# Kernel tuning notes

Measured on AMD Instinct MI355X. Metric: run time of the kernel, lower is better.

## Reference

```python
import jax, jax.numpy as jnp
import numpy as np

N_NODES = 100000
N_EDGES = 1600000
D = 64
H = 128
EPS = 0.0  # learn_eps=False


def setup_inputs() -> dict:
    key = jax.random.key(0)
    k1, k2, k3, k4 = jax.random.split(key, 4)
    x = jax.random.normal(k1, (N_NODES, D), dtype=jnp.float32)
    edge_index = jax.random.randint(k2, (2, N_EDGES), 0, N_NODES, dtype=jnp.int64)
    W1 = jax.random.normal(k3, (D, H), dtype=jnp.float32) * (1.0 / np.sqrt(D))
    b1 = jnp.zeros((H,), dtype=jnp.float32)
    W2 = jax.random.normal(k4, (H, D), dtype=jnp.float32) * (1.0 / np.sqrt(H))
    b2 = jnp.zeros((D,), dtype=jnp.float32)
    return {"x": x, "edge_index": edge_index, "W1": W1, "b1": b1, "W2": W2, "b2": b2}


def reference(x, edge_index, W1, b1, W2, b2):
    src, dst = edge_index[0], edge_index[1]
    # gather neighbor features and scatter-add to destination nodes
    agg = jax.ops.segment_sum(x[src], dst, num_segments=N_NODES)  # [N, D]
    out = agg + (1.0 + EPS) * x
    # GIN MLP: Linear -> ReLU -> Linear
    h = jax.nn.relu(out @ W1 + b1)
    return h @ W2 + b2
```

## Files before the change

kernel.cpp:

```cpp
#include <hip/hip_runtime.h>

#define N_NODES 100000
#define N_EDGES 1600000
#define D 64
#define H 128
#define SCAN_BS 512
#define SCAN_NBLK ((N_NODES + SCAN_BS - 1) / SCAN_BS)

#define NB 1563
#define NCHUNK 256
#define EPC (N_EDGES / NCHUNK)
#define BCAP 2560
#define OVF_CAP 4096

#define MFMA_GRID 512
#define SH_STRIDE 132

typedef __attribute__((ext_vector_type(8))) short short8;
typedef __attribute__((ext_vector_type(4))) float floatx4;
typedef __attribute__((ext_vector_type(4))) unsigned short ushort4_t;

__device__ __forceinline__ unsigned short f2bf(float f) {
    unsigned u = __builtin_bit_cast(unsigned, f);
    u += 0x7FFFu + ((u >> 16) & 1u);
    return (unsigned short)(u >> 16);
}
__device__ __forceinline__ float bf2f(unsigned short u) {
    unsigned v = ((unsigned)u) << 16;
    return __builtin_bit_cast(float, v);
}

__global__ __launch_bounds__(256) void k_zero(int* __restrict__ p, int n) {
    int i = blockIdx.x * 256 + threadIdx.x;
    if (i < n) p[i] = 0;
}

__global__ __launch_bounds__(256) void k_xbf16(const float4* __restrict__ x4,
                                               ushort4_t* __restrict__ y, int n4) {
    int i = blockIdx.x * 256 + threadIdx.x;
    if (i >= n4) return;
    float4 v = x4[i];
    ushort4_t o;
    o[0] = f2bf(v.x); o[1] = f2bf(v.y); o[2] = f2bf(v.z); o[3] = f2bf(v.w);
    y[i] = o;
}

__global__ __launch_bounds__(256) void k_bhist(const int* __restrict__ dst,
                                               int* __restrict__ M2,
                                               int* __restrict__ ovfn) {
    __shared__ int hist[NB];
    int t = threadIdx.x, c = blockIdx.x;
    if (c == 0 && t == 0) ovfn[0] = 0;
    for (int i = t; i < NB; i += 256) hist[i] = 0;
    __syncthreads();
    const int* dp = dst + c * EPC;
    for (int i = t; i < EPC; i += 256) atomicAdd(&hist[dp[i] >> 6], 1);
    __syncthreads();
    int* mp = M2 + c * NB;
    for (int i = t; i < NB; i += 256) mp[i] = hist[i];
}

__global__ __launch_bounds__(256) void k_colscan(int* __restrict__ M2,
                                                 int* __restrict__ colsum) {
    int b = blockIdx.x * 256 + threadIdx.x;
    if (b >= NB) return;
    int run = 0;
    for (int c = 0; c < NCHUNK; c++) {
        int v = M2[c * NB + b];
        M2[c * NB + b] = run;
        run += v;
    }
    colsum[b] = run;
}

__global__ __launch_bounds__(512) void k_bscan(const int* __restrict__ colsum,
                                               int* __restrict__ bends) {
    __shared__ int part[512];
    int t = threadIdx.x;
    int i0 = t * 4;
    int v0 = (i0 + 0 < NB) ? colsum[i0 + 0] : 0;
    int v1 = (i0 + 1 < NB) ? colsum[i0 + 1] : 0;
    int v2 = (i0 + 2 < NB) ? colsum[i0 + 2] : 0;
    int v3 = (i0 + 3 < NB) ? colsum[i0 + 3] : 0;
    int r0 = v0, r1 = r0 + v1, r2 = r1 + v2, r3 = r2 + v3;
    part[t] = r3;
    __syncthreads();
    for (int off = 1; off < 512; off <<= 1) {
        int u = (t >= off) ? part[t - off] : 0;
        __syncthreads();
        part[t] += u;
        __syncthreads();
    }
    int base = (t > 0) ? part[t - 1] : 0;
    if (i0 + 0 < NB) bends[i0 + 0] = base + r0;
    if (i0 + 1 < NB) bends[i0 + 1] = base + r1;
    if (i0 + 2 < NB) bends[i0 + 2] = base + r2;
    if (i0 + 3 < NB) bends[i0 + 3] = base + r3;
}

__global__ __launch_bounds__(256) void k_part(const int* __restrict__ src,
                                              const int* __restrict__ dst,
                                              const int* __restrict__ M2,
                                              const int* __restrict__ bends,
                                              int* __restrict__ ebuf) {
    __shared__ int cur[NB];
    int t = threadIdx.x, c = blockIdx.x;
    const int* mp = M2 + c * NB;
    for (int i = t; i < NB; i += 256)
        cur[i] = ((i > 0) ? bends[i - 1] : 0) + mp[i];
    __syncthreads();
    const int* sp = src + c * EPC;
    const int* dp = dst + c * EPC;
    for (int i = t; i < EPC; i += 256) {
        int d = dp[i], s = sp[i];
        int p = atomicAdd(&cur[d >> 6], 1);
        ebuf[p] = s | ((d & 63) << 17);
    }
}

__global__ __launch_bounds__(256) void k_bagg3(const float* __restrict__ x,
                                               const unsigned short* __restrict__ x16,
                                               const int* __restrict__ ebuf,
                                               const int* __restrict__ bends,
                                               int* __restrict__ ovfn,
                                               int* __restrict__ ovf,
                                               float* __restrict__ out) {
    __shared__ int scur[64];
    __shared__ int snd[64];
    __shared__ int slist[BCAP];
    int t = threadIdx.x, b = blockIdx.x;
    int estart = (b > 0) ? bends[b - 1] : 0;
    int ne = bends[b] - estart;
    const int* ep = ebuf + estart;

    if (t < 64) scur[t] = 0;
    __syncthreads();
    for (int i = t; i < ne; i += 256) atomicAdd(&scur[ep[i] >> 17], 1);
    __syncthreads();
    if (t < 64) {
        int v = scur[t], s = v;
#pragma unroll
        for (int off = 1; off < 64; off <<= 1) {
            int u = __shfl_up(s, off, 64);
            if (t >= off) s += u;
        }
        snd[t] = s;
        scur[t] = s - v;
    }
    __syncthreads();
    for (int i = t; i < ne; i += 256) {
        int v = ep[i];
        int p = atomicAdd(&scur[v >> 17], 1);
        if (p < BCAP) {
            slist[p] = v & 0x1FFFF;
        } else {
            int o = atomicAdd(ovfn, 1);
            if (o < OVF_CAP) { ovf[2 * o] = b * 64 + (v >> 17); ovf[2 * o + 1] = v & 0x1FFFF; }
        }
    }
    __syncthreads();

    int qw = t >> 4;
    int f4 = t & 15;
#pragma unroll
    for (int k = 0; k < 4; k++) {
        int dlow = qw * 4 + k;
        int node = b * 64 + dlow;
        int s0 = (dlow > 0) ? snd[dlow - 1] : 0;
        int e1 = snd[dlow];
        if (s0 > BCAP) s0 = BCAP;
        if (e1 > BCAP) e1 = BCAP;
        float4 a0 = make_float4(0.f, 0.f, 0.f, 0.f);
        float4 a1 = a0, a2 = a0, a3 = a0;
        int i = s0;
        for (; i + 4 <= e1; i += 4) {
            int sA = slist[i], sB = slist[i + 1], sC = slist[i + 2], sD = slist[i + 3];
            ushort4_t uA = *(const ushort4_t*)&x16[(size_t)sA * D + f4 * 4];
            ushort4_t uB = *(const ushort4_t*)&x16[(size_t)sB * D + f4 * 4];
            ushort4_t uC = *(const ushort4_t*)&x16[(size_t)sC * D + f4 * 4];
            ushort4_t uD = *(const ushort4_t*)&x16[(size_t)sD * D + f4 * 4];
            a0.x += bf2f(uA[0]); a0.y += bf2f(uA[1]); a0.z += bf2f(uA[2]); a0.w += bf2f(uA[3]);
            a1.x += bf2f(uB[0]); a1.y += bf2f(uB[1]); a1.z += bf2f(uB[2]); a1.w += bf2f(uB[3]);
            a2.x += bf2f(uC[0]); a2.y += bf2f(uC[1]); a2.z += bf2f(uC[2]); a2.w += bf2f(uC[3]);
            a3.x += bf2f(uD[0]); a3.y += bf2f(uD[1]); a3.z += bf2f(uD[2]); a3.w += bf2f(uD[3]);
        }
        for (; i < e1; i++) {
            int sA = slist[i];
            ushort4_t uA = *(const ushort4_t*)&x16[(size_t)sA * D + f4 * 4];
            a0.x += bf2f(uA[0]); a0.y += bf2f(uA[1]); a0.z += bf2f(uA[2]); a0.w += bf2f(uA[3]);
        }
        a0.x = (a0.x + a1.x) + (a2.x + a3.x);
        a0.y = (a0.y + a1.y) + (a2.y + a3.y);
        a0.z = (a0.z + a1.z) + (a2.z + a3.z);
        a0.w = (a0.w + a1.w) + (a2.w + a3.w);
        if (node < N_NODES) {
            float4 xv = *(const float4*)&x[(size_t)node * D + f4 * 4];
            float4 o;
            o.x = a0.x + xv.x; o.y = a0.y + xv.y; o.z = a0.z + xv.z; o.w = a0.w + xv.w;
            *(float4*)&out[(size_t)node * D + f4 * 4] = o;
        }
    }
}

__global__ __launch_bounds__(256) void k_ovf(const int* __restrict__ ovfn,
                                             const int* __restrict__ ovf,
                                             const float* __restrict__ x,
                                             float* __restrict__ out) {
    int n = *ovfn;
    if (n > OVF_CAP) n = OVF_CAP;
    int f = threadIdx.x & 63;
    for (int idx = threadIdx.x >> 6; idx < n; idx += 4) {
        int d = ovf[2 * idx], s = ovf[2 * idx + 1];
        atomicAdd(&out[(size_t)d * D + f], x[(size_t)s * D + f]);
    }
}

__global__ __launch_bounds__(SCAN_BS) void k_scan1(const int* __restrict__ cnt,
                                                   int* __restrict__ ends,
                                                   int* __restrict__ bsum, int n) {
    __shared__ int s[SCAN_BS];
    int t = threadIdx.x, b = blockIdx.x;
    int id = b * SCAN_BS + t;
    s[t] = (id < n) ? cnt[id] : 0;
    __syncthreads();
    for (int off = 1; off < SCAN_BS; off <<= 1) {
        int u = (t >= off) ? s[t - off] : 0;
        __syncthreads();
        s[t] += u;
        __syncthreads();
    }
    if (id < n) ends[id] = s[t];
    if (t == SCAN_BS - 1) bsum[b] = s[t];
}

__global__ __launch_bounds__(256) void k_scan2(int* __restrict__ bsum, int nb) {
    __shared__ int s[256];
    int t = threadIdx.x;
    s[t] = (t < nb) ? bsum[t] : 0;
    __syncthreads();
    for (int off = 1; off < 256; off <<= 1) {
        int u = (t >= off) ? s[t - off] : 0;
        __syncthreads();
        s[t] += u;
        __syncthreads();
    }
    if (t < nb) bsum[t] = s[t];
}

__global__ __launch_bounds__(SCAN_BS) void k_scan3(int* __restrict__ ends,
                                                   const int* __restrict__ bsum, int n) {
    int t = threadIdx.x, b = blockIdx.x;
    int id = b * SCAN_BS + t;
    if (b > 0 && id < n) ends[id] += bsum[b - 1];
}

__global__ __launch_bounds__(256) void k_histpos(const int* __restrict__ dst,
                                                 int* __restrict__ cnt,
                                                 int* __restrict__ pos) {
    int e = blockIdx.x * 256 + threadIdx.x;
    if (e < N_EDGES) pos[e] = atomicAdd(&cnt[dst[e]], 1);
}

__global__ __launch_bounds__(256) void k_fill2(const int* __restrict__ src,
                                               const int* __restrict__ dst,
                                               const int* __restrict__ pos,
                                               const int* __restrict__ ends,
                                               int* __restrict__ csr) {
    int e = blockIdx.x * 256 + threadIdx.x;
    if (e >= N_EDGES) return;
    int d = dst[e];
    int start = (d > 0) ? ends[d - 1] : 0;
    csr[start + pos[e]] = src[e];
}

__global__ __launch_bounds__(256) void k_agg(const float* __restrict__ x,
                                             const int* __restrict__ csr,
                                             const int* __restrict__ ends,
                                             float* __restrict__ out) {
    int node = blockIdx.x * 4 + (threadIdx.x >> 6);
    if (node >= N_NODES) return;
    int f = threadIdx.x & 63;
    int start = (node > 0) ? ends[node - 1] : 0;
    int end = ends[node];
    float a0 = x[(size_t)node * D + f], a1 = 0.f, a2 = 0.f, a3 = 0.f;
    int e = start;
    for (; e + 4 <= end; e += 4) {
        int s0 = csr[e], s1 = csr[e + 1], s2 = csr[e + 2], s3 = csr[e + 3];
        a0 += x[(size_t)s0 * D + f];
        a1 += x[(size_t)s1 * D + f];
        a2 += x[(size_t)s2 * D + f];
        a3 += x[(size_t)s3 * D + f];
    }
    for (; e < end; e++) a0 += x[(size_t)csr[e] * D + f];
    out[(size_t)node * D + f] = (a0 + a1) + (a2 + a3);
}

__global__ __launch_bounds__(256) void k_init(const float4* __restrict__ x4,
                                              float4* __restrict__ agg4, int n4) {
    int i = blockIdx.x * 256 + threadIdx.x;
    if (i < n4) agg4[i] = x4[i];
}

__global__ __launch_bounds__(256) void k_scatter(const float4* __restrict__ x4,
                                                 const int* __restrict__ src,
                                                 const int* __restrict__ dst,
                                                 float* __restrict__ agg) {
    int gid = blockIdx.x * 256 + threadIdx.x;
    int e = gid >> 4;
    if (e >= N_EDGES) return;
    int c = gid & 15;
    float4 v = x4[src[e] * 16 + c];
    float* p = agg + (size_t)dst[e] * D + c * 4;
    atomicAdd(p + 0, v.x);
    atomicAdd(p + 1, v.y);
    atomicAdd(p + 2, v.z);
    atomicAdd(p + 3, v.w);
}

__global__ __launch_bounds__(256) void k_mlp_mfma(float* __restrict__ io,
                                                  const float* __restrict__ W1,
                                                  const float* __restrict__ b1,
                                                  const float* __restrict__ W2,
                                                  const float* __restrict__ b2) {
    __shared__ unsigned short sW1b[8192];
    __shared__ unsigned short sW2b[8192];
    __shared__ float sh[4][16 * SH_STRIDE];
    __shared__ float sb1[H];
    __shared__ float sb2[D];

    int t = threadIdx.x;

    for (int q = t; q < 8192; q += 256) {
        int j = q & 7, l = (q >> 3) & 63, f = q >> 9;
        int nt = f & 7, kt = f >> 3;
        int k = kt * 32 + ((l >> 4) << 3) + j;
        int n = nt * 16 + (l & 15);
        sW1b[q] = f2bf(W1[k * H + n]);
    }
    for (int q = t; q < 8192; q += 256) {
        int j = q & 7, l = (q >> 3) & 63, f = q >> 9;
        int nt = f & 3, kt = f >> 2;
        int k = kt * 32 + ((l >> 4) << 3) + j;
        int n = nt * 16 + (l & 15);
        sW2b[q] = f2bf(W2[k * D + n]);
    }
    if (t < H) sb1[t] = b1[t];
    if (t >= H && t < H + D) sb2[t - H] = b2[t - H];
    __syncthreads();

    int w = t >> 6, l = t & 63;
    int m = l & 15, q4 = l >> 4;
    float* shw = sh[w];

    const int NT16 = N_NODES / 16;
    const int WAVES = MFMA_GRID * 4;
    const int ITERS = (NT16 + WAVES - 1) / WAVES;

    for (int it = 0; it < ITERS; ++it) {
        int tl = it * WAVES + blockIdx.x * 4 + w;
        bool valid = tl < NT16;
        int nbase = tl * 16;

        if (valid) {
            const float* xr = io + (size_t)(nbase + m) * D + q4 * 8;
            float4 a0 = *(const float4*)(xr);
            float4 a1 = *(const float4*)(xr + 4);
            float4 c0 = *(const float4*)(xr + 32);
            float4 c1 = *(const float4*)(xr + 36);
            short8 A0, A1;
            A0[0] = f2bf(a0.x); A0[1] = f2bf(a0.y); A0[2] = f2bf(a0.z); A0[3] = f2bf(a0.w);
            A0[4] = f2bf(a1.x); A0[5] = f2bf(a1.y); A0[6] = f2bf(a1.z); A0[7] = f2bf(a1.w);
            A1[0] = f2bf(c0.x); A1[1] = f2bf(c0.y); A1[2] = f2bf(c0.z); A1[3] = f2bf(c0.w);
            A1[4] = f2bf(c1.x); A1[5] = f2bf(c1.y); A1[6] = f2bf(c1.z); A1[7] = f2bf(c1.w);

#pragma unroll
            for (int nt = 0; nt < 8; nt++) {
                float bv = sb1[nt * 16 + m];
                floatx4 acc = {bv, bv, bv, bv};
                short8 B0 = *(const short8*)&sW1b[(0 * 8 + nt) * 512 + l * 8];
                short8 B1 = *(const short8*)&sW1b[(1 * 8 + nt) * 512 + l * 8];
                acc = __builtin_amdgcn_mfma_f32_16x16x32_bf16(A0, B0, acc, 0, 0, 0);
                acc = __builtin_amdgcn_mfma_f32_16x16x32_bf16(A1, B1, acc, 0, 0, 0);
#pragma unroll
                for (int r = 0; r < 4; r++)
                    shw[(q4 * 4 + r) * SH_STRIDE + nt * 16 + m] = fmaxf(acc[r], 0.f);
            }
        }
        __syncthreads();

        if (valid) {
            short8 Ah[4];
#pragma unroll
            for (int kt = 0; kt < 4; kt++) {
                const float* hr = &shw[m * SH_STRIDE + kt * 32 + q4 * 8];
                float4 h0 = *(const float4*)(hr);
                float4 h1 = *(const float4*)(hr + 4);
                Ah[kt][0] = f2bf(h0.x); Ah[kt][1] = f2bf(h0.y);
                Ah[kt][2] = f2bf(h0.z); Ah[kt][3] = f2bf(h0.w);
                Ah[kt][4] = f2bf(h1.x); Ah[kt][5] = f2bf(h1.y);
                Ah[kt][6] = f2bf(h1.z); Ah[kt][7] = f2bf(h1.w);
            }
#pragma unroll
            for (int nt = 0; nt < 4; nt++) {
                float bv = sb2[nt * 16 + m];
                floatx4 acc = {bv, bv, bv, bv};
#pragma unroll
                for (int kt = 0; kt < 4; kt++) {
                    short8 B = *(const short8*)&sW2b[(kt * 4 + nt) * 512 + l * 8];
                    acc = __builtin_amdgcn_mfma_f32_16x16x32_bf16(Ah[kt], B, acc, 0, 0, 0);
                }
#pragma unroll
                for (int r = 0; r < 4; r++)
                    io[(size_t)(nbase + q4 * 4 + r) * D + nt * 16 + m] = acc[r];
            }
        }
        __syncthreads();
    }
}

extern "C" void kernel_launch(void* const* d_in, const int* in_sizes, int n_in,
                              void* d_out, int out_size, void* d_ws, size_t ws_size,
                              hipStream_t stream) {
    const float* x  = (const float*)d_in[0];
    const int* eidx = (const int*)d_in[1];
    const float* W1 = (const float*)d_in[2];
    const float* b1 = (const float*)d_in[3];
    const float* W2 = (const float*)d_in[4];
    const float* b2 = (const float*)d_in[5];
    float* out      = (float*)d_out;

    const int* src = eidx;
    const int* dst = eidx + N_EDGES;

    int ge = (N_EDGES + 255) / 256;
    int n4 = N_NODES * D / 4;

    size_t need_A = (size_t)N_NODES * D * sizeof(unsigned short)
                  + (size_t)(N_EDGES + NCHUNK * NB + 2 * NB + 4 + 2 * OVF_CAP) * sizeof(int);
    size_t need_B = (size_t)(2 * N_NODES + 512 + 2 * N_EDGES) * sizeof(int);

    if (ws_size >= need_A) {
        unsigned short* x16 = (unsigned short*)d_ws;
        int* ebuf   = (int*)(x16 + (size_t)N_NODES * D);
        int* M2     = ebuf + N_EDGES;
        int* colsum = M2 + NCHUNK * NB;
        int* bends  = colsum + NB;
        int* ovfn   = bends + NB;
        int* ovf    = ovfn + 4;

        k_xbf16<<<(n4 + 255) / 256, 256, 0, stream>>>((const float4*)x, (ushort4_t*)x16, n4);
        k_bhist<<<NCHUNK, 256, 0, stream>>>(dst, M2, ovfn);
        k_colscan<<<(NB + 255) / 256, 256, 0, stream>>>(M2, colsum);
        k_bscan<<<1, 512, 0, stream>>>(colsum, bends);
        k_part<<<NCHUNK, 256, 0, stream>>>(src, dst, M2, bends, ebuf);
        k_bagg3<<<NB, 256, 0, stream>>>(x, x16, ebuf, bends, ovfn, ovf, out);
        k_ovf<<<1, 256, 0, stream>>>(ovfn, ovf, x, out);
    } else if (ws_size >= need_B) {
        int* cnt  = (int*)d_ws;
        int* ends = cnt + N_NODES;
        int* bsum = ends + N_NODES;
        int* pos  = bsum + 512;
        int* csr  = pos + N_EDGES;

        k_zero<<<(N_NODES + 255) / 256, 256, 0, stream>>>(cnt, N_NODES);
        k_histpos<<<ge, 256, 0, stream>>>(dst, cnt, pos);
        k_scan1<<<SCAN_NBLK, SCAN_BS, 0, stream>>>(cnt, ends, bsum, N_NODES);
        k_scan2<<<1, 256, 0, stream>>>(bsum, SCAN_NBLK);
        k_scan3<<<SCAN_NBLK, SCAN_BS, 0, stream>>>(ends, bsum, N_NODES);
        k_fill2<<<ge, 256, 0, stream>>>(src, dst, pos, ends, csr);
        k_agg<<<(N_NODES + 3) / 4, 256, 0, stream>>>(x, csr, ends, out);
    } else {
        k_init<<<(n4 + 255) / 256, 256, 0, stream>>>((const float4*)x, (float4*)out, n4);
        long long total = (long long)N_EDGES * 16;
        k_scatter<<<(int)((total + 255) / 256), 256, 0, stream>>>(
            (const float4*)x, src, dst, out);
    }

    k_mlp_mfma<<<MFMA_GRID, 256, 0, stream>>>(out, W1, b1, W2, b2);
}
```

Baseline: 195.6 us.

## Store aggregated features as bf16 and fuse preprocessing kernels into one launch

The aggregation kernel now writes its node features as bf16 into a workspace buffer, so the MLP reads half the bytes and skips per-tile conversion. Hidden activations are kept as bf16 in shared memory. The weight conversion and swizzling runs once in a merged preprocessing kernel that also does the edge histogram and the x-to-bf16 conversion, replacing three launches. The aggregation also uses 8-wide bf16 loads, and the MLP grid grows to 768 blocks. In exchange, rounding the aggregate to bf16 before the MLP adds error, and the overflow path now does non-atomic read-modify-write on bf16 values with a single thread block.

```diff
diff --git a/kernel.cpp b/kernel.cpp
--- a/kernel.cpp
+++ b/kernel.cpp
@@ -13,12 +13,14 @@
 #define BCAP 2560
 #define OVF_CAP 4096
 
-#define MFMA_GRID 512
+#define MFMA_GRID 768
 #define SH_STRIDE 132
+#define SH16_ST 136
 
 typedef __attribute__((ext_vector_type(8))) short short8;
 typedef __attribute__((ext_vector_type(4))) float floatx4;
 typedef __attribute__((ext_vector_type(4))) unsigned short ushort4_t;
+typedef __attribute__((ext_vector_type(8))) unsigned short ushort8_t;
 
 __device__ __forceinline__ unsigned short f2bf(float f) {
     unsigned u = __builtin_bit_cast(unsigned, f);
@@ -35,29 +37,53 @@
     if (i < n) p[i] = 0;
 }
 
-__global__ __launch_bounds__(256) void k_xbf16(const float4* __restrict__ x4,
-                                               ushort4_t* __restrict__ y, int n4) {
-    int i = blockIdx.x * 256 + threadIdx.x;
-    if (i >= n4) return;
-    float4 v = x4[i];
-    ushort4_t o;
-    o[0] = f2bf(v.x); o[1] = f2bf(v.y); o[2] = f2bf(v.z); o[3] = f2bf(v.w);
-    y[i] = o;
-}
-
-__global__ __launch_bounds__(256) void k_bhist(const int* __restrict__ dst,
-                                               int* __restrict__ M2,
-                                               int* __restrict__ ovfn) {
+__global__ __launch_bounds__(256) void k_pre(const float4* __restrict__ x4,
+                                             ushort4_t* __restrict__ y, int n4,
+                                             const int* __restrict__ dst,
+                                             int* __restrict__ M2,
+                                             int* __restrict__ ovfn,
+                                             const float* __restrict__ W1,
+                                             const float* __restrict__ W2,
+                                             unsigned short* __restrict__ gW1b,
+                                             unsigned short* __restrict__ gW2b) {
     __shared__ int hist[NB];
-    int t = threadIdx.x, c = blockIdx.x;
-    if (c == 0 && t == 0) ovfn[0] = 0;
-    for (int i = t; i < NB; i += 256) hist[i] = 0;
-    __syncthreads();
-    const int* dp = dst + c * EPC;
-    for (int i = t; i < EPC; i += 256) atomicAdd(&hist[dp[i] >> 6], 1);
-    __syncthreads();
-    int* mp = M2 + c * NB;
-    for (int i = t; i < NB; i += 256) mp[i] = hist[i];
+    int t = threadIdx.x, blk = blockIdx.x;
+    if (blk < NCHUNK) {
+        int c = blk;
+        if (c == 0 && t == 0) ovfn[0] = 0;
+        for (int i = t; i < NB; i += 256) hist[i] = 0;
+        __syncthreads();
+        const int* dp = dst + c * EPC;
+        for (int i = t; i < EPC; i += 256) atomicAdd(&hist[dp[i] >> 6], 1);
+        __syncthreads();
+        int* mp = M2 + c * NB;
+        for (int i = t; i < NB; i += 256) mp[i] = hist[i];
+    } else if (blk == NCHUNK) {
+        for (int q = t; q < 8192; q += 256) {
+            int j = q & 7, l = (q >> 3) & 63, f = q >> 9;
+            int nt = f & 7, kt = f >> 3;
+            int k = kt * 32 + ((l >> 4) << 3) + j;
+            int n = nt * 16 + (l & 15);
+            gW1b[q] = f2bf(W1[k * H + n]);
+        }
+    } else if (blk == NCHUNK + 1) {
+        for (int q = t; q < 8192; q += 256) {
+            int j = q & 7, l = (q >> 3) & 63, f = q >> 9;
+            int nt = f & 3, kt = f >> 2;
+            int k = kt * 32 + ((l >> 4) << 3) + j;
+            int n = nt * 16 + (l & 15);
+            gW2b[q] = f2bf(W2[k * D + n]);
+        }
+    } else {
+        int cb = blk - NCHUNK - 2;
+        int nconv = gridDim.x - NCHUNK - 2;
+        for (int i = cb * 256 + t; i < n4; i += nconv * 256) {
+            float4 v = x4[i];
+            ushort4_t o;
+            o[0] = f2bf(v.x); o[1] = f2bf(v.y); o[2] = f2bf(v.z); o[3] = f2bf(v.w);
+            y[i] = o;
+        }
+    }
 }
 
 __global__ __launch_bounds__(256) void k_colscan(int* __restrict__ M2,
@@ -118,13 +144,13 @@
     }
 }
 
-__global__ __launch_bounds__(256) void k_bagg3(const float* __restrict__ x,
+__global__ __launch_bounds__(256) void k_bagg4(const float* __restrict__ x,
                                                const unsigned short* __restrict__ x16,
                                                const int* __restrict__ ebuf,
                                                const int* __restrict__ bends,
                                                int* __restrict__ ovfn,
                                                int* __restrict__ ovf,
-                                               float* __restrict__ out) {
+                                               unsigned short* __restrict__ o16) {
     __shared__ int scur[64];
     __shared__ int snd[64];
     __shared__ int slist[BCAP];
@@ -160,58 +186,248 @@
     }
     __syncthreads();
 
-    int qw = t >> 4;
-    int f4 = t & 15;
-#pragma unroll
-    for (int k = 0; k < 4; k++) {
-        int dlow = qw * 4 + k;
+    int g = t >> 3;
+    int l8 = t & 7;
+#pragma unroll
+    for (int k = 0; k < 2; k++) {
+        int dlow = g * 2 + k;
         int node = b * 64 + dlow;
         int s0 = (dlow > 0) ? snd[dlow - 1] : 0;
         int e1 = snd[dlow];
         if (s0 > BCAP) s0 = BCAP;
         if (e1 > BCAP) e1 = BCAP;
-        float4 a0 = make_float4(0.f, 0.f, 0.f, 0.f);
-        float4 a1 = a0, a2 = a0, a3 = a0;
+        float accA[8], accB[8];
+#pragma unroll
+        for (int j = 0; j < 8; j++) { accA[j] = 0.f; accB[j] = 0.f; }
         int i = s0;
         for (; i + 4 <= e1; i += 4) {
             int sA = slist[i], sB = slist[i + 1], sC = slist[i + 2], sD = slist[i + 3];
-            ushort4_t uA = *(const ushort4_t*)&x16[(size_t)sA * D + f4 * 4];
-            ushort4_t uB = *(const ushort4_t*)&x16[(size_t)sB * D + f4 * 4];
-            ushort4_t uC = *(const ushort4_t*)&x16[(size_t)sC * D + f4 * 4];
-            ushort4_t uD = *(const ushort4_t*)&x16[(size_t)sD * D + f4 * 4];
-            a0.x += bf2f(uA[0]); a0.y += bf2f(uA[1]); a0.z += bf2f(uA[2]); a0.w += bf2f(uA[3]);
-            a1.x += bf2f(uB[0]); a1.y += bf2f(uB[1]); a1.z += bf2f(uB[2]); a1.w += bf2f(uB[3]);
-            a2.x += bf2f(uC[0]); a2.y += bf2f(uC[1]); a2.z += bf2f(uC[2]); a2.w += bf2f(uC[3]);
-            a3.x += bf2f(uD[0]); a3.y += bf2f(uD[1]); a3.z += bf2f(uD[2]); a3.w += bf2f(uD[3]);
+            ushort8_t uA = *(const ushort8_t*)&x16[(size_t)sA * D + l8 * 8];
+            ushort8_t uB = *(const ushort8_t*)&x16[(size_t)sB * D + l8 * 8];
+            ushort8_t uC = *(const ushort8_t*)&x16[(size_t)sC * D + l8 * 8];
+            ushort8_t uD = *(const ushort8_t*)&x16[(size_t)sD * D + l8 * 8];
+#pragma unroll
+            for (int j = 0; j < 8; j++) accA[j] += bf2f(uA[j]);
+#pragma unroll
+            for (int j = 0; j < 8; j++) accB[j] += bf2f(uB[j]);
+#pragma unroll
+            for (int j = 0; j < 8; j++) accA[j] += bf2f(uC[j]);
+#pragma unroll
+            for (int j = 0; j < 8; j++) accB[j] += bf2f(uD[j]);
         }
         for (; i < e1; i++) {
             int sA = slist[i];
-            ushort4_t uA = *(const ushort4_t*)&x16[(size_t)sA * D + f4 * 4];
-            a0.x += bf2f(uA[0]); a0.y += bf2f(uA[1]); a0.z += bf2f(uA[2]); a0.w += bf2f(uA[3]);
-        }
-        a0.x = (a0.x + a1.x) + (a2.x + a3.x);
-        a0.y = (a0.y + a1.y) + (a2.y + a3.y);
-        a0.z = (a0.z + a1.z) + (a2.z + a3.z);
-        a0.w = (a0.w + a1.w) + (a2.w + a3.w);
+            ushort8_t uA = *(const ushort8_t*)&x16[(size_t)sA * D + l8 * 8];
+#pragma unroll
+            for (int j = 0; j < 8; j++) accA[j] += bf2f(uA[j]);
+        }
         if (node < N_NODES) {
-            float4 xv = *(const float4*)&x[(size_t)node * D + f4 * 4];
-            float4 o;
-            o.x = a0.x + xv.x; o.y = a0.y + xv.y; o.z = a0.z + xv.z; o.w = a0.w + xv.w;
-            *(float4*)&out[(size_t)node * D + f4 * 4] = o;
-        }
-    }
-}
-
-__global__ __launch_bounds__(256) void k_ovf(const int* __restrict__ ovfn,
-                                             const int* __restrict__ ovf,
-                                             const float* __restrict__ x,
-                                             float* __restrict__ out) {
+            const float* xp = x + (size_t)node * D + l8 * 8;
+            float4 x0 = *(const float4*)xp;
+            float4 x1 = *(const float4*)(xp + 4);
+            ushort8_t o;
+            o[0] = f2bf(accA[0] + accB[0] + x0.x);
+            o[1] = f2bf(accA[1] + accB[1] + x0.y);
+            o[2] = f2bf(accA[2] + accB[2] + x0.z);
+            o[3] = f2bf(accA[3] + accB[3] + x0.w);
+            o[4] = f2bf(accA[4] + accB[4] + x1.x);
+            o[5] = f2bf(accA[5] + accB[5] + x1.y);
+            o[6] = f2bf(accA[6] + accB[6] + x1.z);
+            o[7] = f2bf(accA[7] + accB[7] + x1.w);
+            *(ushort8_t*)&o16[(size_t)node * D + l8 * 8] = o;
+        }
+    }
+}
+
+__global__ __launch_bounds__(64) void k_ovf(const int* __restrict__ ovfn,
+                                            const int* __restrict__ ovf,
+                                            const float* __restrict__ x,
+                                            unsigned short* __restrict__ o16) {
     int n = *ovfn;
     if (n > OVF_CAP) n = OVF_CAP;
-    int f = threadIdx.x & 63;
-    for (int idx = threadIdx.x >> 6; idx < n; idx += 4) {
+    int f = threadIdx.x;
+    for (int idx = 0; idx < n; idx++) {
         int d = ovf[2 * idx], s = ovf[2 * idx + 1];
-        atomicAdd(&out[(size_t)d * D + f], x[(size_t)s * D + f]);
+        unsigned short* p = &o16[(size_t)d * D + f];
+        *p = f2bf(bf2f(*p) + x[(size_t)s * D + f]);
+    }
+}
+
+__global__ __launch_bounds__(256) void k_mlp16(const unsigned short* __restrict__ in16,
+                                               float* __restrict__ outp,
+                                               const unsigned short* __restrict__ gW1b,
+                                               const unsigned short* __restrict__ gW2b,
+                                               const float* __restrict__ b1,
+                                               const float* __restrict__ b2) {
+    __shared__ unsigned short sW1b[8192];
+    __shared__ unsigned short sW2b[8192];
+    __shared__ unsigned short sh16[4][16 * SH16_ST];
+    __shared__ float sb1[H];
+    __shared__ float sb2[D];
+
+    int t = threadIdx.x;
+    for (int q = t; q < 1024; q += 256) {
+        *(short8*)&sW1b[q * 8] = *(const short8*)&gW1b[q * 8];
+        *(short8*)&sW2b[q * 8] = *(const short8*)&gW2b[q * 8];
+    }
+    if (t < H) sb1[t] = b1[t];
+    if (t >= H && t < H + D) sb2[t - H] = b2[t - H];
+    __syncthreads();
+
+    int w = t >> 6, l = t & 63;
+    int m = l & 15, q4 = l >> 4;
+    unsigned short* shw = sh16[w];
+
+    const int NT16 = N_NODES / 16;
+    const int WAVES = MFMA_GRID * 4;
+    const int ITERS = (NT16 + WAVES - 1) / WAVES;
+
+    for (int it = 0; it < ITERS; ++it) {
+        int tl = it * WAVES + blockIdx.x * 4 + w;
+        bool valid = tl < NT16;
+        int nbase = tl * 16;
+
+        if (valid) {
+            const unsigned short* xr = in16 + (size_t)(nbase + m) * D + q4 * 8;
+            short8 A0 = *(const short8*)(xr);
+            short8 A1 = *(const short8*)(xr + 32);
+
+#pragma unroll
+            for (int nt = 0; nt < 8; nt++) {
+                float bv = sb1[nt * 16 + m];
+                floatx4 acc = {bv, bv, bv, bv};
+                short8 B0 = *(const short8*)&sW1b[(0 * 8 + nt) * 512 + l * 8];
+                short8 B1 = *(const short8*)&sW1b[(1 * 8 + nt) * 512 + l * 8];
+                acc = __builtin_amdgcn_mfma_f32_16x16x32_bf16(A0, B0, acc, 0, 0, 0);
+                acc = __builtin_amdgcn_mfma_f32_16x16x32_bf16(A1, B1, acc, 0, 0, 0);
+#pragma unroll
+                for (int r = 0; r < 4; r++)
+                    shw[(q4 * 4 + r) * SH16_ST + nt * 16 + m] = f2bf(fmaxf(acc[r], 0.f));
+            }
+        }
+        __syncthreads();
+
+        if (valid) {
+            short8 Ah[4];
+#pragma unroll
+            for (int kt = 0; kt < 4; kt++)
+                Ah[kt] = *(const short8*)&shw[m * SH16_ST + kt * 32 + q4 * 8];
+#pragma unroll
+            for (int nt = 0; nt < 4; nt++) {
+                float bv = sb2[nt * 16 + m];
+                floatx4 acc = {bv, bv, bv, bv};
+#pragma unroll
+                for (int kt = 0; kt < 4; kt++) {
+                    short8 B = *(const short8*)&sW2b[(kt * 4 + nt) * 512 + l * 8];
+                    acc = __builtin_amdgcn_mfma_f32_16x16x32_bf16(Ah[kt], B, acc, 0, 0, 0);
+                }
+#pragma unroll
+                for (int r = 0; r < 4; r++)
+                    outp[(size_t)(nbase + q4 * 4 + r) * D + nt * 16 + m] = acc[r];
+            }
+        }
+        __syncthreads();
+    }
+}
+
+__global__ __launch_bounds__(256) void k_mlp_f32(float* __restrict__ io,
+                                                 const float* __restrict__ W1,
+                                                 const float* __restrict__ b1,
+                                                 const float* __restrict__ W2,
+                                                 const float* __restrict__ b2) {
+    __shared__ unsigned short sW1b[8192];
+    __shared__ unsigned short sW2b[8192];
+    __shared__ float sh[4][16 * SH_STRIDE];
+    __shared__ float sb1[H];
+    __shared__ float sb2[D];
+
+    int t = threadIdx.x;
+
+    for (int q = t; q < 8192; q += 256) {
+        int j = q & 7, l = (q >> 3) & 63, f = q >> 9;
+        int nt = f & 7, kt = f >> 3;
+        int k = kt * 32 + ((l >> 4) << 3) + j;
+        int n = nt * 16 + (l & 15);
+        sW1b[q] = f2bf(W1[k * H + n]);
+    }
+    for (int q = t; q < 8192; q += 256) {
+        int j = q & 7, l = (q >> 3) & 63, f = q >> 9;
+        int nt = f & 3, kt = f >> 2;
+        int k = kt * 32 + ((l >> 4) << 3) + j;
+        int n = nt * 16 + (l & 15);
+        sW2b[q] = f2bf(W2[k * D + n]);
+    }
+    if (t < H) sb1[t] = b1[t];
+    if (t >= H && t < H + D) sb2[t - H] = b2[t - H];
+    __syncthreads();
+
+    int w = t >> 6, l = t & 63;
+    int m = l & 15, q4 = l >> 4;
+    float* shw = sh[w];
+
+    const int NT16 = N_NODES / 16;
+    const int WAVES = 512 * 4;
+    const int ITERS = (NT16 + WAVES - 1) / WAVES;
+
+    for (int it = 0; it < ITERS; ++it) {
+        int tl = it * WAVES + blockIdx.x * 4 + w;
+        bool valid = tl < NT16;
+        int nbase = tl * 16;
+
+        if (valid) {
+            const float* xr = io + (size_t)(nbase + m) * D + q4 * 8;
+            float4 a0 = *(const float4*)(xr);
+            float4 a1 = *(const float4*)(xr + 4);
+            float4 c0 = *(const float4*)(xr + 32);
+            float4 c1 = *(const float4*)(xr + 36);
+            short8 A0, A1;
+            A0[0] = f2bf(a0.x); A0[1] = f2bf(a0.y); A0[2] = f2bf(a0.z); A0[3] = f2bf(a0.w);
+            A0[4] = f2bf(a1.x); A0[5] = f2bf(a1.y); A0[6] = f2bf(a1.z); A0[7] = f2bf(a1.w);
+            A1[0] = f2bf(c0.x); A1[1] = f2bf(c0.y); A1[2] = f2bf(c0.z); A1[3] = f2bf(c0.w);
+            A1[4] = f2bf(c1.x); A1[5] = f2bf(c1.y); A1[6] = f2bf(c1.z); A1[7] = f2bf(c1.w);
+
+#pragma unroll
+            for (int nt = 0; nt < 8; nt++) {
+                float bv = sb1[nt * 16 + m];
+                floatx4 acc = {bv, bv, bv, bv};
+                short8 B0 = *(const short8*)&sW1b[(0 * 8 + nt) * 512 + l * 8];
+                short8 B1 = *(const short8*)&sW1b[(1 * 8 + nt) * 512 + l * 8];
+                acc = __builtin_amdgcn_mfma_f32_16x16x32_bf16(A0, B0, acc, 0, 0, 0);
+                acc = __builtin_amdgcn_mfma_f32_16x16x32_bf16(A1, B1, acc, 0, 0, 0);
+#pragma unroll
+                for (int r = 0; r < 4; r++)
+                    shw[(q4 * 4 + r) * SH_STRIDE + nt * 16 + m] = fmaxf(acc[r], 0.f);
+            }
+        }
+        __syncthreads();
+
+        if (valid) {
+            short8 Ah[4];
+#pragma unroll
+            for (int kt = 0; kt < 4; kt++) {
+                const float* hr = &shw[m * SH_STRIDE + kt * 32 + q4 * 8];
+                float4 h0 = *(const float4*)(hr);
+                float4 h1 = *(const float4*)(hr + 4);
+                Ah[kt][0] = f2bf(h0.x); Ah[kt][1] = f2bf(h0.y);
+                Ah[kt][2] = f2bf(h0.z); Ah[kt][3] = f2bf(h0.w);
+                Ah[kt][4] = f2bf(h1.x); Ah[kt][5] = f2bf(h1.y);
+                Ah[kt][6] = f2bf(h1.z); Ah[kt][7] = f2bf(h1.w);
+            }
+#pragma unroll
+            for (int nt = 0; nt < 4; nt++) {
+                float bv = sb2[nt * 16 + m];
+                floatx4 acc = {bv, bv, bv, bv};
+#pragma unroll
+                for (int kt = 0; kt < 4; kt++) {
+                    short8 B = *(const short8*)&sW2b[(kt * 4 + nt) * 512 + l * 8];
+                    acc = __builtin_amdgcn_mfma_f32_16x16x32_bf16(Ah[kt], B, acc, 0, 0, 0);
+                }
+#pragma unroll
+                for (int r = 0; r < 4; r++)
+                    io[(size_t)(nbase + q4 * 4 + r) * D + nt * 16 + m] = acc[r];
+            }
+        }
+        __syncthreads();
     }
 }
 
@@ -317,107 +533,6 @@
     atomicAdd(p + 3, v.w);
 }
 
-__global__ __launch_bounds__(256) void k_mlp_mfma(float* __restrict__ io,
-                                                  const float* __restrict__ W1,
-                                                  const float* __restrict__ b1,
-                                                  const float* __restrict__ W2,
-                                                  const float* __restrict__ b2) {
-    __shared__ unsigned short sW1b[8192];
-    __shared__ unsigned short sW2b[8192];
-    __shared__ float sh[4][16 * SH_STRIDE];
-    __shared__ float sb1[H];
-    __shared__ float sb2[D];
-
-    int t = threadIdx.x;
-
-    for (int q = t; q < 8192; q += 256) {
-        int j = q & 7, l = (q >> 3) & 63, f = q >> 9;
-        int nt = f & 7, kt = f >> 3;
-        int k = kt * 32 + ((l >> 4) << 3) + j;
-        int n = nt * 16 + (l & 15);
-        sW1b[q] = f2bf(W1[k * H + n]);
-    }
-    for (int q = t; q < 8192; q += 256) {
-        int j = q & 7, l = (q >> 3) & 63, f = q >> 9;
-        int nt = f & 3, kt = f >> 2;
-        int k = kt * 32 + ((l >> 4) << 3) + j;
-        int n = nt * 16 + (l & 15);
-        sW2b[q] = f2bf(W2[k * D + n]);
-    }
-    if (t < H) sb1[t] = b1[t];
-    if (t >= H && t < H + D) sb2[t - H] = b2[t - H];
-    __syncthreads();
-
-    int w = t >> 6, l = t & 63;
-    int m = l & 15, q4 = l >> 4;
-    float* shw = sh[w];
-
-    const int NT16 = N_NODES / 16;
-    const int WAVES = MFMA_GRID * 4;
-    const int ITERS = (NT16 + WAVES - 1) / WAVES;
-
-    for (int it = 0; it < ITERS; ++it) {
-        int tl = it * WAVES + blockIdx.x * 4 + w;
-        bool valid = tl < NT16;
-        int nbase = tl * 16;
-
-        if (valid) {
-            const float* xr = io + (size_t)(nbase + m) * D + q4 * 8;
-            float4 a0 = *(const float4*)(xr);
-            float4 a1 = *(const float4*)(xr + 4);
-            float4 c0 = *(const float4*)(xr + 32);
-            float4 c1 = *(const float4*)(xr + 36);
-            short8 A0, A1;
-            A0[0] = f2bf(a0.x); A0[1] = f2bf(a0.y); A0[2] = f2bf(a0.z); A0[3] = f2bf(a0.w);
-            A0[4] = f2bf(a1.x); A0[5] = f2bf(a1.y); A0[6] = f2bf(a1.z); A0[7] = f2bf(a1.w);
-            A1[0] = f2bf(c0.x); A1[1] = f2bf(c0.y); A1[2] = f2bf(c0.z); A1[3] = f2bf(c0.w);
-            A1[4] = f2bf(c1.x); A1[5] = f2bf(c1.y); A1[6] = f2bf(c1.z); A1[7] = f2bf(c1.w);
-
-#pragma unroll
-            for (int nt = 0; nt < 8; nt++) {
-                float bv = sb1[nt * 16 + m];
-                floatx4 acc = {bv, bv, bv, bv};
-                short8 B0 = *(const short8*)&sW1b[(0 * 8 + nt) * 512 + l * 8];
-                short8 B1 = *(const short8*)&sW1b[(1 * 8 + nt) * 512 + l * 8];
-                acc = __builtin_amdgcn_mfma_f32_16x16x32_bf16(A0, B0, acc, 0, 0, 0);
-                acc = __builtin_amdgcn_mfma_f32_16x16x32_bf16(A1, B1, acc, 0, 0, 0);
-#pragma unroll
-                for (int r = 0; r < 4; r++)
-                    shw[(q4 * 4 + r) * SH_STRIDE + nt * 16 + m] = fmaxf(acc[r], 0.f);
-            }
-        }
-        __syncthreads();
-
-        if (valid) {
-            short8 Ah[4];
-#pragma unroll
-            for (int kt = 0; kt < 4; kt++) {
-                const float* hr = &shw[m * SH_STRIDE + kt * 32 + q4 * 8];
-                float4 h0 = *(const float4*)(hr);
-                float4 h1 = *(const float4*)(hr + 4);
-                Ah[kt][0] = f2bf(h0.x); Ah[kt][1] = f2bf(h0.y);
-                Ah[kt][2] = f2bf(h0.z); Ah[kt][3] = f2bf(h0.w);
-                Ah[kt][4] = f2bf(h1.x); Ah[kt][5] = f2bf(h1.y);
-                Ah[kt][6] = f2bf(h1.z); Ah[kt][7] = f2bf(h1.w);
-            }
-#pragma unroll
-            for (int nt = 0; nt < 4; nt++) {
-                float bv = sb2[nt * 16 + m];
-                floatx4 acc = {bv, bv, bv, bv};
-#pragma unroll
-                for (int kt = 0; kt < 4; kt++) {
-                    short8 B = *(const short8*)&sW2b[(kt * 4 + nt) * 512 + l * 8];
-                    acc = __builtin_amdgcn_mfma_f32_16x16x32_bf16(Ah[kt], B, acc, 0, 0, 0);
-                }
-#pragma unroll
-                for (int r = 0; r < 4; r++)
-                    io[(size_t)(nbase + q4 * 4 + r) * D + nt * 16 + m] = acc[r];
-            }
-        }
-        __syncthreads();
-    }
-}
-
 extern "C" void kernel_launch(void* const* d_in, const int* in_sizes, int n_in,
                               void* d_out, int out_size, void* d_ws, size_t ws_size,
                               hipStream_t stream) {
@@ -435,26 +550,31 @@
     int ge = (N_EDGES + 255) / 256;
     int n4 = N_NODES * D / 4;
 
-    size_t need_A = (size_t)N_NODES * D * sizeof(unsigned short)
-                  + (size_t)(N_EDGES + NCHUNK * NB + 2 * NB + 4 + 2 * OVF_CAP) * sizeof(int);
+    size_t need_A = (size_t)N_NODES * D * 2 * sizeof(unsigned short)
+                  + (size_t)(N_EDGES + NCHUNK * NB + 2 * NB + 4 + 2 * OVF_CAP) * sizeof(int)
+                  + (size_t)16384 * sizeof(unsigned short);
     size_t need_B = (size_t)(2 * N_NODES + 512 + 2 * N_EDGES) * sizeof(int);
 
     if (ws_size >= need_A) {
         unsigned short* x16 = (unsigned short*)d_ws;
-        int* ebuf   = (int*)(x16 + (size_t)N_NODES * D);
+        unsigned short* o16 = x16 + (size_t)N_NODES * D;
+        int* ebuf   = (int*)(o16 + (size_t)N_NODES * D);
         int* M2     = ebuf + N_EDGES;
         int* colsum = M2 + NCHUNK * NB;
         int* bends  = colsum + NB;
         int* ovfn   = bends + NB;
         int* ovf    = ovfn + 4;
-
-        k_xbf16<<<(n4 + 255) / 256, 256, 0, stream>>>((const float4*)x, (ushort4_t*)x16, n4);
-        k_bhist<<<NCHUNK, 256, 0, stream>>>(dst, M2, ovfn);
+        unsigned short* gW1b = (unsigned short*)(ovf + 2 * OVF_CAP);
+        unsigned short* gW2b = gW1b + 8192;
+
+        k_pre<<<NCHUNK + 2 + 2048, 256, 0, stream>>>((const float4*)x, (ushort4_t*)x16, n4,
+                                                     dst, M2, ovfn, W1, W2, gW1b, gW2b);
         k_colscan<<<(NB + 255) / 256, 256, 0, stream>>>(M2, colsum);
         k_bscan<<<1, 512, 0, stream>>>(colsum, bends);
         k_part<<<NCHUNK, 256, 0, stream>>>(src, dst, M2, bends, ebuf);
-        k_bagg3<<<NB, 256, 0, stream>>>(x, x16, ebuf, bends, ovfn, ovf, out);
-        k_ovf<<<1, 256, 0, stream>>>(ovfn, ovf, x, out);
+        k_bagg4<<<NB, 256, 0, stream>>>(x, x16, ebuf, bends, ovfn, ovf, o16);
+        k_ovf<<<1, 64, 0, stream>>>(ovfn, ovf, x, o16);
+        k_mlp16<<<MFMA_GRID, 256, 0, stream>>>(o16, out, gW1b, gW2b, b1, b2);
     } else if (ws_size >= need_B) {
         int* cnt  = (int*)d_ws;
         int* ends = cnt + N_NODES;
@@ -469,12 +589,12 @@
         k_scan3<<<SCAN_NBLK, SCAN_BS, 0, stream>>>(ends, bsum, N_NODES);
         k_fill2<<<ge, 256, 0, stream>>>(src, dst, pos, ends, csr);
         k_agg<<<(N_NODES + 3) / 4, 256, 0, stream>>>(x, csr, ends, out);
+        k_mlp_f32<<<512, 256, 0, stream>>>(out, W1, b1, W2, b2);
     } else {
         k_init<<<(n4 + 255) / 256, 256, 0, stream>>>((const float4*)x, (float4*)out, n4);
         long long total = (long long)N_EDGES * 16;
         k_scatter<<<(int)((total + 255) / 256), 256, 0, stream>>>(
             (const float4*)x, src, dst, out);
-    }
-
-    k_mlp_mfma<<<MFMA_GRID, 256, 0, stream>>>(out, W1, b1, W2, b2);
-}
+        k_mlp_f32<<<512, 256, 0, stream>>>(out, W1, b1, W2, b2);
+    }
+}
```

Measured after the change: 176.9 us. 9.6% less time.
